# Kernel tuning notes

Hardware: AMD Instinct MI355X
Metric: run time of the kernel (lower is better)

The kernel has to match this reference:

```python
import jax, jax.numpy as jnp
import numpy as np

B, S, HID = 1, 2048, 2048
NH, NKV = 16, 4
HD = HID // NH  # 128


def _rope_manual(x, cos_h, sin_h):
    # x: [B, S, nh, HD]; cos_h/sin_h: [1, S, 1, HD//2]
    d = x.shape[-1]
    x_rot = x[..., : d // 2]
    x_pass = x[..., d // 2:]
    # rotate interleaved pairs inside the first half
    x_rot = jnp.stack([-x_rot[..., 1::2], x_rot[..., ::2]], axis=-1)
    x_rot = x_rot.reshape(x_rot.shape[:-2] + (d // 2,))
    return jnp.concatenate(
        [x_rot * cos_h + x_pass * sin_h, -x_rot * sin_h + x_pass * cos_h], axis=-1
    )


def setup_inputs() -> dict:
    key = jax.random.key(0)
    ks = jax.random.split(key, 7)
    bound = 1.0 / np.sqrt(HID)
    return {
        "x": jax.random.normal(ks[0], (B, S, HID), jnp.float32),
        "cos": jax.random.uniform(ks[1], (S, HD), jnp.float32),
        "sin": jax.random.uniform(ks[2], (S, HD), jnp.float32),
        "wq": jax.random.uniform(ks[3], (NH * HD, HID), jnp.float32, -bound, bound),
        "wk": jax.random.uniform(ks[4], (NKV * HD, HID), jnp.float32, -bound, bound),
        "wv": jax.random.uniform(ks[5], (NKV * HD, HID), jnp.float32, -bound, bound),
        "wo": jax.random.uniform(ks[6], (HID, HID), jnp.float32, -bound, bound),
    }


def reference(x, cos, sin, wq, wk, wv, wo):
    b, s, _ = x.shape
    q = jnp.einsum("bsh,oh->bso", x, wq).reshape(b, s, NH, HD)
    k = jnp.einsum("bsh,oh->bso", x, wk).reshape(b, s, NKV, HD)
    v = jnp.einsum("bsh,oh->bso", x, wv).reshape(b, s, NKV, HD)

    cos_h = cos[None, :, None, : HD // 2]  # [1,S,1,HD/2]
    sin_h = sin[None, :, None, : HD // 2]
    q = _rope_manual(q, cos_h, sin_h)
    k = _rope_manual(k, cos_h, sin_h)

    # [B, H, S, D]
    q = q.transpose(0, 2, 1, 3)
    k = k.transpose(0, 2, 1, 3)
    v = v.transpose(0, 2, 1, 3)
    # GQA kv repeat (repeat_interleave over head dim)
    rep = NH // NKV
    k = jnp.repeat(k, rep, axis=1)
    v = jnp.repeat(v, rep, axis=1)

    scale = 1.0 / np.sqrt(HD).astype(np.float32)
    scores = jnp.einsum("bhqd,bhkd->bhqk", q, k) * scale
    causal = jnp.tril(jnp.ones((s, s), bool))
    scores = jnp.where(causal[None, None], scores, jnp.finfo(scores.dtype).min)
    attn = jax.nn.softmax(scores, axis=-1)
    out = jnp.einsum("bhqk,bhkd->bhqd", attn, v)  # [B,H,S,D]
    out = out.transpose(0, 2, 1, 3).reshape(b, s, NH * HD)
    return jnp.einsum("bso,ho->bsh", out, wo)
```

## Files before the change

### kernel.cpp

```cpp
#include <hip/hip_runtime.h>
#include <hip/hip_bf16.h>

typedef __bf16 bf16_t;
typedef __attribute__((ext_vector_type(8))) __bf16 bf16x8;
typedef __attribute__((ext_vector_type(4))) __bf16 bf16x4;
typedef __attribute__((ext_vector_type(4))) float f32x4;

#define S_LEN 2048
#define HID 2048
#define NH 16
#define NKV 4
#define HD 128

__device__ __forceinline__ void gll16(const bf16_t* g, bf16_t* l) {
    __builtin_amdgcn_global_load_lds(
        (const __attribute__((address_space(1))) unsigned int*)g,
        (__attribute__((address_space(3))) unsigned int*)l, 16, 0, 0);
}

__device__ __forceinline__ bf16x8 cvt2x4(float4 a, float4 b) {
    bf16x8 o;
    o[0]=(bf16_t)a.x; o[1]=(bf16_t)a.y; o[2]=(bf16_t)a.z; o[3]=(bf16_t)a.w;
    o[4]=(bf16_t)b.x; o[5]=(bf16_t)b.y; o[6]=(bf16_t)b.z; o[7]=(bf16_t)b.w;
    return o;
}

__global__ __launch_bounds__(256) void cvt_f32_bf16(const float* __restrict__ in,
                                                    bf16_t* __restrict__ out, int n)
{
    int i = (blockIdx.x * 256 + threadIdx.x) * 8;
    if (i >= n) return;
    float4 a = *(const float4*)&in[i];
    float4 b = *(const float4*)&in[i + 4];
    *(bf16x8*)&out[i] = cvt2x4(a, b);
}

__global__ __launch_bounds__(256) void cvt_w3(const float* __restrict__ wq,
                                              const float* __restrict__ wk,
                                              const float* __restrict__ wv,
                                              bf16_t* __restrict__ out)
{
    int i = (blockIdx.x * 256 + threadIdx.x) * 8;
    const float* src; int off;
    if (i < 4 * 1024 * 1024)      { src = wq; off = i; }
    else if (i < 5 * 1024 * 1024) { src = wk; off = i - 4 * 1024 * 1024; }
    else                          { src = wv; off = i - 5 * 1024 * 1024; }
    float4 a = *(const float4*)&src[off];
    float4 b = *(const float4*)&src[off + 4];
    *(bf16x8*)&out[i] = cvt2x4(a, b);
}

template<int MODE, typename CT>
__global__ __launch_bounds__(256, 2) void gemm128(
    const bf16_t* __restrict__ A, const bf16_t* __restrict__ B,
    CT* __restrict__ C, bf16_t* __restrict__ CkP, bf16_t* __restrict__ CvtP,
    int N, int K)
{
    __shared__ __align__(16) bf16_t sA[128 * 64];
    __shared__ __align__(16) bf16_t sB[128 * 64];

    const int tid = threadIdx.x, lane = tid & 63, wave = tid >> 6;
    const int l16 = lane & 15, quad = lane >> 4;
    const int m0 = blockIdx.y * 128, n0 = blockIdx.x * 128;
    const int wm = (wave >> 1) * 64, wn = (wave & 1) * 64;

    const bf16_t* gA[4]; const bf16_t* gB[4];
    bf16_t* lA[4]; bf16_t* lB[4];
#pragma unroll
    for (int t = 0; t < 4; t++) {
        int p = (wave * 4 + t) * 64 + lane;
        int row = p >> 3;
        int lc = (p & 7) ^ (row & 7);
        gA[t] = A + (size_t)(m0 + row) * K + lc * 8;
        gB[t] = B + (size_t)(n0 + row) * K + lc * 8;
        lA[t] = &sA[(wave * 4 + t) * 512];
        lB[t] = &sB[(wave * 4 + t) * 512];
    }

    int offA[2][4], offB[2][4];
#pragma unroll
    for (int kc = 0; kc < 2; kc++)
#pragma unroll
        for (int i = 0; i < 4; i++) {
            int rm = wm + i * 16 + l16;
            offA[kc][i] = rm * 64 + (((kc * 4 + quad) ^ (rm & 7)) * 8);
            int rn = wn + i * 16 + l16;
            offB[kc][i] = rn * 64 + (((kc * 4 + quad) ^ (rn & 7)) * 8);
        }

    f32x4 acc[4][4] = {};

    for (int k0 = 0; k0 < K; k0 += 64) {
        __syncthreads();
#pragma unroll
        for (int t = 0; t < 4; t++) {
            gll16(gA[t], lA[t]);
            gll16(gB[t], lB[t]);
            gA[t] += 64; gB[t] += 64;
        }
        __syncthreads();

#pragma unroll
        for (int kc = 0; kc < 2; kc++) {
            bf16x8 af[4], bfv[4];
#pragma unroll
            for (int i = 0; i < 4; i++) af[i] = *(bf16x8*)&sA[offA[kc][i]];
#pragma unroll
            for (int j = 0; j < 4; j++) bfv[j] = *(bf16x8*)&sB[offB[kc][j]];
#pragma unroll
            for (int i = 0; i < 4; i++)
#pragma unroll
                for (int j = 0; j < 4; j++)
                    acc[i][j] = __builtin_amdgcn_mfma_f32_16x16x32_bf16(af[i], bfv[j], acc[i][j], 0, 0, 0);
        }
    }

#pragma unroll
    for (int i = 0; i < 4; i++) {
        int rowb = m0 + wm + i * 16 + quad * 4;
#pragma unroll
        for (int j = 0; j < 4; j++) {
            int col = n0 + wn + j * 16 + l16;
#pragma unroll
            for (int r = 0; r < 4; r++) {
                float v = acc[i][j][r];
                int row = rowb + r;
                if (MODE == 0) {
                    C[(size_t)row * N + col] = (CT)v;
                } else {
                    if (col < 2048)      C[(size_t)row * 2048 + col] = (CT)v;
                    else if (col < 2560) CkP[(size_t)row * 512 + (col - 2048)] = (bf16_t)v;
                    else                 CvtP[(size_t)(col - 2560) * S_LEN + row] = (bf16_t)v;
                }
            }
        }
    }
}

__global__ void rope_all(bf16_t* __restrict__ Qh, bf16_t* __restrict__ Kh,
                         const float* __restrict__ cosb, const float* __restrict__ sinb)
{
    int s = blockIdx.x;
    int grp = blockIdx.y;
    int sub = threadIdx.x >> 5;
    int i = threadIdx.x & 31;
    bf16_t* row = (grp < 4) ? (Qh + ((size_t)s * NH + grp * 4 + sub) * HD)
                            : (Kh + ((size_t)s * NKV + sub) * HD);
    float x0 = (float)row[2 * i];
    float x1 = (float)row[2 * i + 1];
    float p0 = (float)row[64 + 2 * i];
    float p1 = (float)row[64 + 2 * i + 1];
    float c0 = cosb[s * HD + 2 * i];
    float c1 = cosb[s * HD + 2 * i + 1];
    float n0 = sinb[s * HD + 2 * i];
    float n1 = sinb[s * HD + 2 * i + 1];
    float r0 = -x1, r1 = x0;
    row[2 * i]          = (bf16_t)(r0 * c0 + p0 * n0);
    row[2 * i + 1]      = (bf16_t)(r1 * c1 + p1 * n1);
    row[64 + 2 * i]     = (bf16_t)(-r0 * n0 + p0 * c0);
    row[64 + 2 * i + 1] = (bf16_t)(-r1 * n1 + p1 * c1);
}

__global__ __launch_bounds__(256, 1) void flash_attn5(
    const bf16_t* __restrict__ Q,
    const bf16_t* __restrict__ Kb,
    const bf16_t* __restrict__ VT,
    bf16_t* __restrict__ Opart,
    float* __restrict__ lpart,
    int S)
{
    __shared__ __align__(16) bf16_t sK[64 * 136];
    __shared__ __align__(16) bf16_t sVT[128 * 72];
    __shared__ __align__(16) bf16_t sP[4][16 * 72];

    const int qt  = blockIdx.x;
    const int kvh = blockIdx.y;
    const int z   = blockIdx.z;
    const int h0  = kvh * 4;
    const int q0  = qt * 64;
    const int tid = threadIdx.x, lane = tid & 63, wave = tid >> 6;
    const int l16 = lane & 15, quad = lane >> 4;
    const float scale = 0.08838834764831845f;

    const int nkt = qt + 1;
    const int h0c = nkt >> 1;
    const int tb  = z ? h0c : 0;
    const int te  = z ? nkt : h0c;

    const int qrow = q0 + wave * 16 + l16;

    bf16x8 qf[4][4];
#pragma unroll
    for (int h = 0; h < 4; h++)
#pragma unroll
        for (int c = 0; c < 4; c++)
            qf[h][c] = *(const bf16x8*)&Q[(size_t)qrow * HID + (h0 + h) * HD + c * 32 + quad * 8];

    f32x4 oacc[4][8] = {};
    float lsum[4] = {0.f, 0.f, 0.f, 0.f};

    int krow[4], kcol[4], vrow[4], vcol[4];
#pragma unroll
    for (int it = 0; it < 4; it++) {
        int c = tid + 256 * it;
        krow[it] = c >> 4; kcol[it] = (c & 15) * 8;
        vrow[it] = c >> 3; vcol[it] = (c & 7) * 8;
    }

    bf16x8 kpre[4], vpre[4];
#pragma unroll
    for (int it = 0; it < 4; it++) {
        kpre[it] = *(const bf16x8*)&Kb[(size_t)(tb * 64 + krow[it]) * (NKV * HD) + kvh * HD + kcol[it]];
        vpre[it] = *(const bf16x8*)&VT[((size_t)kvh * HD + vrow[it]) * S + tb * 64 + vcol[it]];
    }

    for (int kt = tb; kt < te; kt++) {
        const int t0 = kt * 64;
        __syncthreads();
#pragma unroll
        for (int it = 0; it < 4; it++) {
            *(bf16x8*)&sK[krow[it] * 136 + kcol[it]] = kpre[it];
            *(bf16x8*)&sVT[vrow[it] * 72 + vcol[it]] = vpre[it];
        }
        __syncthreads();

        if (kt + 1 < te) {
            const int t1 = t0 + 64;
#pragma unroll
            for (int it = 0; it < 4; it++) {
                kpre[it] = *(const bf16x8*)&Kb[(size_t)(t1 + krow[it]) * (NKV * HD) + kvh * HD + kcol[it]];
                vpre[it] = *(const bf16x8*)&VT[((size_t)kvh * HD + vrow[it]) * S + t1 + vcol[it]];
            }
        }

        f32x4 sc[4][4];
#pragma unroll
        for (int nt = 0; nt < 4; nt++) {
            bf16x8 kf[4];
#pragma unroll
            for (int c = 0; c < 4; c++)
                kf[c] = *(bf16x8*)&sK[(nt * 16 + l16) * 136 + c * 32 + quad * 8];
#pragma unroll
            for (int h = 0; h < 4; h++) {
                f32x4 d = {};
#pragma unroll
                for (int c = 0; c < 4; c++)
                    d = __builtin_amdgcn_mfma_f32_16x16x32_bf16(kf[c], qf[h][c], d, 0, 0, 0);
                sc[h][nt] = d;
            }
        }

        bf16x8 pa[4][2];
#pragma unroll
        for (int h = 0; h < 4; h++) {
#pragma unroll
            for (int nt = 0; nt < 4; nt++) {
                const int tbk = t0 + nt * 16 + quad * 4;
                bf16x4 pk;
#pragma unroll
                for (int r = 0; r < 4; r++) {
                    float p = (tbk + r <= qrow) ? __expf(sc[h][nt][r] * scale) : 0.0f;
                    lsum[h] += p;
                    pk[r] = (bf16_t)p;
                }
                *(bf16x4*)&sP[wave][l16 * 72 + nt * 16 + quad * 4] = pk;
            }
#pragma unroll
            for (int kc = 0; kc < 2; kc++)
                pa[h][kc] = *(bf16x8*)&sP[wave][l16 * 72 + kc * 32 + quad * 8];
        }

#pragma unroll
        for (int dt = 0; dt < 8; dt++)
#pragma unroll
            for (int kc = 0; kc < 2; kc++) {
                bf16x8 vf = *(bf16x8*)&sVT[(dt * 16 + l16) * 72 + kc * 32 + quad * 8];
#pragma unroll
                for (int h = 0; h < 4; h++)
                    oacc[h][dt] = __builtin_amdgcn_mfma_f32_16x16x32_bf16(pa[h][kc], vf, oacc[h][dt], 0, 0, 0);
            }
    }

    bf16_t* Op = Opart + (size_t)z * S * HID;
#pragma unroll
    for (int h = 0; h < 4; h++) {
        float lr = lsum[h];
        lr += __shfl_xor(lr, 16, 64);
        lr += __shfl_xor(lr, 32, 64);
        if (quad == 0)
            lpart[((size_t)z * S + q0 + wave * 16 + l16) * NH + (h0 + h)] = lr;
#pragma unroll
        for (int r = 0; r < 4; r++) {
            int srow = q0 + wave * 16 + quad * 4 + r;
#pragma unroll
            for (int dt = 0; dt < 8; dt++)
                Op[(size_t)srow * HID + (h0 + h) * HD + dt * 16 + l16] =
                    (bf16_t)(oacc[h][dt][r]);
        }
    }
}

__global__ __launch_bounds__(256) void flash_combine(
    const bf16_t* __restrict__ Opart, const float* __restrict__ lpart,
    bf16_t* __restrict__ oh)
{
    int i = (blockIdx.x * 256 + threadIdx.x) * 8;
    int s = i >> 11;
    int h = (i >> 7) & 15;
    float l = lpart[(size_t)s * NH + h] + lpart[((size_t)S_LEN + s) * NH + h];
    float inv = 1.0f / l;
    bf16x8 a = *(const bf16x8*)&Opart[i];
    bf16x8 b = *(const bf16x8*)&Opart[(size_t)S_LEN * HID + i];
    bf16x8 o;
#pragma unroll
    for (int j = 0; j < 8; j++)
        o[j] = (bf16_t)(((float)a[j] + (float)b[j]) * inv);
    *(bf16x8*)&oh[i] = o;
}

extern "C" void kernel_launch(void* const* d_in, const int* in_sizes, int n_in,
                              void* d_out, int out_size, void* d_ws, size_t ws_size,
                              hipStream_t stream)
{
    const float* x    = (const float*)d_in[0];
    const float* cosb = (const float*)d_in[1];
    const float* sinb = (const float*)d_in[2];
    const float* wq   = (const float*)d_in[3];
    const float* wk   = (const float*)d_in[4];
    const float* wv   = (const float*)d_in[5];
    const float* wo   = (const float*)d_in[6];
    float* out = (float*)d_out;

    char* ws = (char*)d_ws;
    bf16_t* wb = (bf16_t*)(ws);
    bf16_t* qh = (bf16_t*)(ws + (size_t)12 * 1024 * 1024);
    bf16_t* kh = (bf16_t*)(ws + (size_t)20 * 1024 * 1024);
    bf16_t* vT = (bf16_t*)(ws + (size_t)22 * 1024 * 1024);
    float*  lp = (float*) (ws + (size_t)24 * 1024 * 1024);
    bf16_t* xb = (bf16_t*)d_out;
    bf16_t* op = (bf16_t*)d_out;

    const int NX = S_LEN * HID;

    cvt_f32_bf16<<<NX / (256 * 8), 256, 0, stream>>>(x, xb, NX);

    cvt_w3<<<6 * 1024 * 1024 / (256 * 8), 256, 0, stream>>>(wq, wk, wv, wb);

    gemm128<1, bf16_t><<<dim3(24, 16), 256, 0, stream>>>(xb, wb, qh, kh, vT, 3072, HID);

    rope_all<<<dim3(S_LEN, 5), 128, 0, stream>>>(qh, kh, cosb, sinb);

    flash_attn5<<<dim3(32, NKV, 2), 256, 0, stream>>>(qh, kh, vT, op, lp, S_LEN);

    flash_combine<<<NX / (256 * 8), 256, 0, stream>>>(op, lp, qh);

    cvt_f32_bf16<<<NX / (256 * 8), 256, 0, stream>>>(wo, wb, NX);

    gemm128<0, float><<<dim3(16, 16), 256, 0, stream>>>(qh, wb, out, nullptr, nullptr, HID, HID);
}
```

Before: 247.7 us.

## Split long causal query tiles four ways to balance flash-attention work

Flash attention now launches a flat grid of 96 blocks per KV head. The first 16 query tiles split their key range in two and the last 16 split it in four, instead of every tile splitting in two. This should shorten the longest blocks under the causal triangle and raise the block count from 256 to 384 to fill more CUs. The extra partials for the upper half are written into the weight workspace and summed in the combine kernel, which costs more partial-output traffic and a divergent branch in the combine.

```diff
diff --git a/kernel.cpp b/kernel.cpp
--- a/kernel.cpp
+++ b/kernel.cpp
@@ -161,11 +161,12 @@
     row[64 + 2 * i + 1] = (bf16_t)(-r1 * n1 + p1 * c1);
 }
 
-__global__ __launch_bounds__(256, 1) void flash_attn5(
+__global__ __launch_bounds__(256, 1) void flash_attn6(
     const bf16_t* __restrict__ Q,
     const bf16_t* __restrict__ Kb,
     const bf16_t* __restrict__ VT,
-    bf16_t* __restrict__ Opart,
+    bf16_t* __restrict__ OpLo,
+    bf16_t* __restrict__ OpHi,
     float* __restrict__ lpart,
     int S)
 {
@@ -173,9 +174,12 @@
     __shared__ __align__(16) bf16_t sVT[128 * 72];
     __shared__ __align__(16) bf16_t sP[4][16 * 72];
 
-    const int qt  = blockIdx.x;
+    const int bx = blockIdx.x;
+    int qt, z, nsplit;
+    if (bx < 32) { qt = bx >> 1;        z = bx & 1; nsplit = 2; }
+    else         { qt = 16 + ((bx - 32) >> 2); z = (bx - 32) & 3; nsplit = 4; }
+
     const int kvh = blockIdx.y;
-    const int z   = blockIdx.z;
     const int h0  = kvh * 4;
     const int q0  = qt * 64;
     const int tid = threadIdx.x, lane = tid & 63, wave = tid >> 6;
@@ -183,9 +187,8 @@
     const float scale = 0.08838834764831845f;
 
     const int nkt = qt + 1;
-    const int h0c = nkt >> 1;
-    const int tb  = z ? h0c : 0;
-    const int te  = z ? nkt : h0c;
+    const int tb  = (z * nkt) / nsplit;
+    const int te  = ((z + 1) * nkt) / nsplit;
 
     const int qrow = q0 + wave * 16 + l16;
 
@@ -281,7 +284,11 @@
             }
     }
 
-    bf16_t* Op = Opart + (size_t)z * S * HID;
+    bf16_t* Op;
+    int rbase;
+    if (z < 2) { Op = OpLo + (size_t)z * S * HID;            rbase = q0; }
+    else       { Op = OpHi + (size_t)(z - 2) * 1024 * HID;   rbase = q0 - 1024; }
+
 #pragma unroll
     for (int h = 0; h < 4; h++) {
         float lr = lsum[h];
@@ -291,30 +298,40 @@
             lpart[((size_t)z * S + q0 + wave * 16 + l16) * NH + (h0 + h)] = lr;
 #pragma unroll
         for (int r = 0; r < 4; r++) {
-            int srow = q0 + wave * 16 + quad * 4 + r;
+            int prow = rbase + wave * 16 + quad * 4 + r;
 #pragma unroll
             for (int dt = 0; dt < 8; dt++)
-                Op[(size_t)srow * HID + (h0 + h) * HD + dt * 16 + l16] =
+                Op[(size_t)prow * HID + (h0 + h) * HD + dt * 16 + l16] =
                     (bf16_t)(oacc[h][dt][r]);
         }
     }
 }
 
 __global__ __launch_bounds__(256) void flash_combine(
-    const bf16_t* __restrict__ Opart, const float* __restrict__ lpart,
-    bf16_t* __restrict__ oh)
+    const bf16_t* __restrict__ OpLo, const bf16_t* __restrict__ OpHi,
+    const float* __restrict__ lpart, bf16_t* __restrict__ oh)
 {
     int i = (blockIdx.x * 256 + threadIdx.x) * 8;
     int s = i >> 11;
     int h = (i >> 7) & 15;
     float l = lpart[(size_t)s * NH + h] + lpart[((size_t)S_LEN + s) * NH + h];
+    bf16x8 a = *(const bf16x8*)&OpLo[i];
+    bf16x8 b = *(const bf16x8*)&OpLo[(size_t)S_LEN * HID + i];
+    float v[8];
+#pragma unroll
+    for (int j = 0; j < 8; j++) v[j] = (float)a[j] + (float)b[j];
+    if (s >= 1024) {
+        l += lpart[((size_t)2 * S_LEN + s) * NH + h] + lpart[((size_t)3 * S_LEN + s) * NH + h];
+        size_t ih = (size_t)i - (size_t)1024 * HID;
+        bf16x8 c = *(const bf16x8*)&OpHi[ih];
+        bf16x8 d = *(const bf16x8*)&OpHi[(size_t)1024 * HID + ih];
+#pragma unroll
+        for (int j = 0; j < 8; j++) v[j] += (float)c[j] + (float)d[j];
+    }
     float inv = 1.0f / l;
-    bf16x8 a = *(const bf16x8*)&Opart[i];
-    bf16x8 b = *(const bf16x8*)&Opart[(size_t)S_LEN * HID + i];
     bf16x8 o;
 #pragma unroll
-    for (int j = 0; j < 8; j++)
-        o[j] = (bf16_t)(((float)a[j] + (float)b[j]) * inv);
+    for (int j = 0; j < 8; j++) o[j] = (bf16_t)(v[j] * inv);
     *(bf16x8*)&oh[i] = o;
 }
 
@@ -337,8 +354,9 @@
     bf16_t* kh = (bf16_t*)(ws + (size_t)20 * 1024 * 1024);
     bf16_t* vT = (bf16_t*)(ws + (size_t)22 * 1024 * 1024);
     float*  lp = (float*) (ws + (size_t)24 * 1024 * 1024);
-    bf16_t* xb = (bf16_t*)d_out;
-    bf16_t* op = (bf16_t*)d_out;
+    bf16_t* xb   = (bf16_t*)d_out;
+    bf16_t* opLo = (bf16_t*)d_out;
+    bf16_t* opHi = wb;
 
     const int NX = S_LEN * HID;
 
@@ -350,9 +368,9 @@
 
     rope_all<<<dim3(S_LEN, 5), 128, 0, stream>>>(qh, kh, cosb, sinb);
 
-    flash_attn5<<<dim3(32, NKV, 2), 256, 0, stream>>>(qh, kh, vT, op, lp, S_LEN);
-
-    flash_combine<<<NX / (256 * 8), 256, 0, stream>>>(op, lp, qh);
+    flash_attn6<<<dim3(96, NKV), 256, 0, stream>>>(qh, kh, vT, opLo, opHi, lp, S_LEN);
+
+    flash_combine<<<NX / (256 * 8), 256, 0, stream>>>(opLo, opHi, lp, qh);
 
     cvt_f32_bf16<<<NX / (256 * 8), 256, 0, stream>>>(wo, wb, NX);
 
```

New measurement: 253.3 us. 2.3% more time.

## Double-buffer K/V tiles in LDS and skip causal mask off the diagonal

Applied to the files above, without the earlier changes.

Moves the flash attention kernel to double-buffered shared memory for the K and V^T tiles. Each iteration writes the next tile into the alternate buffer and issues global loads two tiles ahead, so the loop needs one barrier instead of two. It also drops the per-element causal comparison on every tile except the diagonal one. The cost is twice the LDS footprint for K and V, plus extra register pressure from the duplicated softmax code.

```diff
diff --git a/kernel.cpp b/kernel.cpp
--- a/kernel.cpp
+++ b/kernel.cpp
@@ -161,7 +161,7 @@
     row[64 + 2 * i + 1] = (bf16_t)(-r1 * n1 + p1 * c1);
 }
 
-__global__ __launch_bounds__(256, 1) void flash_attn5(
+__global__ __launch_bounds__(256, 1) void flash_attn7(
     const bf16_t* __restrict__ Q,
     const bf16_t* __restrict__ Kb,
     const bf16_t* __restrict__ VT,
@@ -169,8 +169,8 @@
     float* __restrict__ lpart,
     int S)
 {
-    __shared__ __align__(16) bf16_t sK[64 * 136];
-    __shared__ __align__(16) bf16_t sVT[128 * 72];
+    __shared__ __align__(16) bf16_t sK[2][64 * 136];
+    __shared__ __align__(16) bf16_t sVT[2][128 * 72];
     __shared__ __align__(16) bf16_t sP[4][16 * 72];
 
     const int qt  = blockIdx.x;
@@ -183,9 +183,9 @@
     const float scale = 0.08838834764831845f;
 
     const int nkt = qt + 1;
-    const int h0c = nkt >> 1;
-    const int tb  = z ? h0c : 0;
-    const int te  = z ? nkt : h0c;
+    const int hc  = nkt >> 1;
+    const int tb  = z ? hc : 0;
+    const int te  = z ? nkt : hc;
 
     const int qrow = q0 + wave * 16 + l16;
 
@@ -213,23 +213,39 @@
         kpre[it] = *(const bf16x8*)&Kb[(size_t)(tb * 64 + krow[it]) * (NKV * HD) + kvh * HD + kcol[it]];
         vpre[it] = *(const bf16x8*)&VT[((size_t)kvh * HD + vrow[it]) * S + tb * 64 + vcol[it]];
     }
-
+#pragma unroll
+    for (int it = 0; it < 4; it++) {
+        *(bf16x8*)&sK[0][krow[it] * 136 + kcol[it]] = kpre[it];
+        *(bf16x8*)&sVT[0][vrow[it] * 72 + vcol[it]] = vpre[it];
+    }
+    if (tb + 1 < te) {
+        const int t1 = (tb + 1) * 64;
+#pragma unroll
+        for (int it = 0; it < 4; it++) {
+            kpre[it] = *(const bf16x8*)&Kb[(size_t)(t1 + krow[it]) * (NKV * HD) + kvh * HD + kcol[it]];
+            vpre[it] = *(const bf16x8*)&VT[((size_t)kvh * HD + vrow[it]) * S + t1 + vcol[it]];
+        }
+    }
+    __syncthreads();
+
+    int sel = 0;
     for (int kt = tb; kt < te; kt++) {
         const int t0 = kt * 64;
-        __syncthreads();
-#pragma unroll
-        for (int it = 0; it < 4; it++) {
-            *(bf16x8*)&sK[krow[it] * 136 + kcol[it]] = kpre[it];
-            *(bf16x8*)&sVT[vrow[it] * 72 + vcol[it]] = vpre[it];
-        }
-        __syncthreads();
+        const int ns = sel ^ 1;
 
         if (kt + 1 < te) {
-            const int t1 = t0 + 64;
 #pragma unroll
             for (int it = 0; it < 4; it++) {
-                kpre[it] = *(const bf16x8*)&Kb[(size_t)(t1 + krow[it]) * (NKV * HD) + kvh * HD + kcol[it]];
-                vpre[it] = *(const bf16x8*)&VT[((size_t)kvh * HD + vrow[it]) * S + t1 + vcol[it]];
+                *(bf16x8*)&sK[ns][krow[it] * 136 + kcol[it]] = kpre[it];
+                *(bf16x8*)&sVT[ns][vrow[it] * 72 + vcol[it]] = vpre[it];
+            }
+            if (kt + 2 < te) {
+                const int t2 = t0 + 128;
+#pragma unroll
+                for (int it = 0; it < 4; it++) {
+                    kpre[it] = *(const bf16x8*)&Kb[(size_t)(t2 + krow[it]) * (NKV * HD) + kvh * HD + kcol[it]];
+                    vpre[it] = *(const bf16x8*)&VT[((size_t)kvh * HD + vrow[it]) * S + t2 + vcol[it]];
+                }
             }
         }
 
@@ -239,7 +255,7 @@
             bf16x8 kf[4];
 #pragma unroll
             for (int c = 0; c < 4; c++)
-                kf[c] = *(bf16x8*)&sK[(nt * 16 + l16) * 136 + c * 32 + quad * 8];
+                kf[c] = *(bf16x8*)&sK[sel][(nt * 16 + l16) * 136 + c * 32 + quad * 8];
 #pragma unroll
             for (int h = 0; h < 4; h++) {
                 f32x4 d = {};
@@ -251,34 +267,57 @@
         }
 
         bf16x8 pa[4][2];
-#pragma unroll
-        for (int h = 0; h < 4; h++) {
-#pragma unroll
-            for (int nt = 0; nt < 4; nt++) {
-                const int tbk = t0 + nt * 16 + quad * 4;
-                bf16x4 pk;
-#pragma unroll
-                for (int r = 0; r < 4; r++) {
-                    float p = (tbk + r <= qrow) ? __expf(sc[h][nt][r] * scale) : 0.0f;
-                    lsum[h] += p;
-                    pk[r] = (bf16_t)p;
+        if (kt == qt) {
+#pragma unroll
+            for (int h = 0; h < 4; h++) {
+#pragma unroll
+                for (int nt = 0; nt < 4; nt++) {
+                    const int tbk = t0 + nt * 16 + quad * 4;
+                    bf16x4 pk;
+#pragma unroll
+                    for (int r = 0; r < 4; r++) {
+                        float p = (tbk + r <= qrow) ? __expf(sc[h][nt][r] * scale) : 0.0f;
+                        lsum[h] += p;
+                        pk[r] = (bf16_t)p;
+                    }
+                    *(bf16x4*)&sP[wave][l16 * 72 + nt * 16 + quad * 4] = pk;
                 }
-                *(bf16x4*)&sP[wave][l16 * 72 + nt * 16 + quad * 4] = pk;
-            }
-#pragma unroll
-            for (int kc = 0; kc < 2; kc++)
-                pa[h][kc] = *(bf16x8*)&sP[wave][l16 * 72 + kc * 32 + quad * 8];
+#pragma unroll
+                for (int kc = 0; kc < 2; kc++)
+                    pa[h][kc] = *(bf16x8*)&sP[wave][l16 * 72 + kc * 32 + quad * 8];
+            }
+        } else {
+#pragma unroll
+            for (int h = 0; h < 4; h++) {
+#pragma unroll
+                for (int nt = 0; nt < 4; nt++) {
+                    bf16x4 pk;
+#pragma unroll
+                    for (int r = 0; r < 4; r++) {
+                        float p = __expf(sc[h][nt][r] * scale);
+                        lsum[h] += p;
+                        pk[r] = (bf16_t)p;
+                    }
+                    *(bf16x4*)&sP[wave][l16 * 72 + nt * 16 + quad * 4] = pk;
+                }
+#pragma unroll
+                for (int kc = 0; kc < 2; kc++)
+                    pa[h][kc] = *(bf16x8*)&sP[wave][l16 * 72 + kc * 32 + quad * 8];
+            }
         }
 
 #pragma unroll
         for (int dt = 0; dt < 8; dt++)
 #pragma unroll
             for (int kc = 0; kc < 2; kc++) {
-                bf16x8 vf = *(bf16x8*)&sVT[(dt * 16 + l16) * 72 + kc * 32 + quad * 8];
+                bf16x8 vf = *(bf16x8*)&sVT[sel][(dt * 16 + l16) * 72 + kc * 32 + quad * 8];
 #pragma unroll
                 for (int h = 0; h < 4; h++)
                     oacc[h][dt] = __builtin_amdgcn_mfma_f32_16x16x32_bf16(pa[h][kc], vf, oacc[h][dt], 0, 0, 0);
             }
+
+        __syncthreads();
+        sel = ns;
     }
 
     bf16_t* Op = Opart + (size_t)z * S * HID;
@@ -350,7 +389,7 @@
 
     rope_all<<<dim3(S_LEN, 5), 128, 0, stream>>>(qh, kh, cosb, sinb);
 
-    flash_attn5<<<dim3(32, NKV, 2), 256, 0, stream>>>(qh, kh, vT, op, lp, S_LEN);
+    flash_attn7<<<dim3(32, NKV, 2), 256, 0, stream>>>(qh, kh, vT, op, lp, S_LEN);
 
     flash_combine<<<NX / (256 * 8), 256, 0, stream>>>(op, lp, qh);
 
```

Measured after the change: 248.9 us. About the same (+0.5%).
